# Kernel optimization log

Hardware: AMD Instinct MI355X
Metric: run time of the kernel (lower is better)

The kernel has to match this reference:

```python
import jax, jax.numpy as jnp
import numpy as np

B, T, S, O, U = 512, 1024, 64, 32, 16


def setup_inputs() -> dict:
    key = jax.random.key(0)
    ks = jax.random.split(key, 6)
    obs = jax.random.normal(ks[0], (B, T, O), jnp.float32)
    inputs = jax.random.normal(ks[1], (B, T, U), jnp.float32)
    # Stable transition matrix: spectral radius < 1 so the recursion doesn't blow up
    A = 0.9 * jnp.eye(S, dtype=jnp.float32) + (0.05 / np.sqrt(S)) * jax.random.normal(ks[2], (S, S), jnp.float32)
    B_mat = 0.1 * jax.random.normal(ks[3], (S, U), jnp.float32)
    C = jax.random.normal(ks[4], (O, S), jnp.float32) / np.sqrt(S)
    Q = jnp.eye(S, dtype=jnp.float32)  # module default when Q not provided
    R = jnp.eye(O, dtype=jnp.float32)  # module default when R not provided
    x0 = jax.random.normal(ks[5], (S,), jnp.float32)
    return dict(obs=obs, inputs=inputs, A=A, B_mat=B_mat, C=C, Q=Q, R=R, x0=x0)


def reference(obs, inputs, A, B_mat, C, Q, R, x0):
    b = obs.shape[0]
    s = A.shape[0]
    I_S = jnp.eye(s, dtype=obs.dtype)
    x_init = jnp.broadcast_to(x0, (b, s))            # initial_state_mean repeated over batch
    P_init = jnpp = jnp.broadcast_to(I_S, (b, s, s))  # P[:,0] = I

    def step(carry, zs):
        x, P = carry          # x: [b,S], P: [b,S,S]
        z, u = zs             # z: [b,O], u: [b,U]
        # stage 1: predict
        x_prior = x @ A.T + u @ B_mat.T                       # [b,S]
        P_prior = jnp.einsum('ij,bjk,lk->bil', A, P, A) + Q   # A P A^T + Q
        # stage 2: measurement update
        S_inn = jnp.einsum('ij,bjk,lk->bil', C, P_prior, C) + R   # [b,O,O]
        K = jnp.einsum('bij,kj,bkl->bil', P_prior, C, jnp.linalg.inv(S_inn))  # [b,S,O]
        innov = z - x_prior @ C.T                              # [b,O]
        x_post = x_prior + jnp.einsum('bij,bj->bi', K, innov)  # [b,S]
        P_post = (I_S - jnp.einsum('bij,jk->bik', K, C)) @ P_prior
        return (x_post, P_post), x_post

    xs = (jnp.swapaxes(obs, 0, 1), jnp.swapaxes(inputs, 0, 1))  # time-major
    _, x_seq = jax.lax.scan(step, (x_init, P_init), xs)          # [T,b,S]
    states_est = jnp.concatenate([x_init[:, None, :], jnp.swapaxes(x_seq, 0, 1)], axis=1)  # [b,T+1,S]
    return states_est
```

## Files before the change

kernel.cpp:

```cpp
#include <hip/hip_runtime.h>

#define NS 64
#define NO 32
#define NU 16
#define NT 1024
#define NB 512
#define TCAP 192
#define GROW 112
#define GROW4 28

#define OFF_A    0
#define OFF_AT   4096
#define OFF_C    8192
#define OFF_CT   10240
#define OFF_CA   12288
#define OFF_CB   14336
#define OFF_B    14848
#define OFF_Q    15872
#define OFF_R    19968
#define OFF_P    20992
#define OFF_PP   25088
#define OFF_X    29184
#define OFF_X2   33280
#define OFF_CP   35328
#define OFF_K    37376
#define OFF_DB   39424
#define LDS_FLOATS 39456

#define FMA4(acc, s, v) do { float4 _v = (v); float _s = (s); \
  acc.x = fmaf(_s,_v.x,acc.x); acc.y = fmaf(_s,_v.y,acc.y); \
  acc.z = fmaf(_s,_v.z,acc.z); acc.w = fmaf(_s,_v.w,acc.w); } while(0)
#define FNM4(acc, s, v) do { float4 _v = (v); float _s = -(s); \
  acc.x = fmaf(_s,_v.x,acc.x); acc.y = fmaf(_s,_v.y,acc.y); \
  acc.z = fmaf(_s,_v.z,acc.z); acc.w = fmaf(_s,_v.w,acc.w); } while(0)

#define GJ_STEP(SRC, DST, KK) do { \
  const float* _s = (SRC); float* _d = (DST); const int _k = (KK); \
  float prcp = 1.0f / _s[_k*64 + _k]; \
  float f  = _s[gi*64 + _k] * prcp; \
  float p0 = _s[_k*64 + gj],      p1 = _s[_k*64 + 16 + gj]; \
  float p2 = _s[_k*64 + 32 + gj], p3 = _s[_k*64 + 48 + gj]; \
  float x0 = _s[gi*64 + gj],      x1 = _s[gi*64 + 16 + gj]; \
  float x2 = _s[gi*64 + 32 + gj], x3 = _s[gi*64 + 48 + gj]; \
  bool piv = (gi == _k); \
  _d[gi*64 + gj]      = piv ? x0 : fmaf(-f, p0, x0); \
  _d[gi*64 + 16 + gj] = piv ? x1 : fmaf(-f, p1, x1); \
  _d[gi*64 + 32 + gj] = piv ? x2 : fmaf(-f, p2, x2); \
  _d[gi*64 + 48 + gj] = piv ? x3 : fmaf(-f, p3, x3); \
} while(0)

__global__ __launch_bounds__(512) void riccati_kernel(
    const float* __restrict__ Ag, const float* __restrict__ Bg,
    const float* __restrict__ Cg, const float* __restrict__ Qg,
    const float* __restrict__ Rg, float* __restrict__ Gout,
    int* __restrict__ hdr, int tcap)
{
  extern __shared__ float sm[];
  float* Al  = sm + OFF_A;
  float* Atl = sm + OFF_AT;
  float* Cl  = sm + OFF_C;
  float* CTl = sm + OFF_CT;
  float* CAl = sm + OFF_CA;
  float* CBl = sm + OFF_CB;
  float* Bl  = sm + OFF_B;
  float* Ql  = sm + OFF_Q;
  float* Rl  = sm + OFF_R;
  float* Pl  = sm + OFF_P;
  float* Ppl = sm + OFF_PP;
  float* Xl  = sm + OFF_X;
  float* X2l = sm + OFF_X2;
  float* CPl = sm + OFF_CP;
  float* Kl  = sm + OFF_K;
  float* db  = sm + OFF_DB;
  __shared__ unsigned redmax;
  __shared__ int done;

  const int tid = threadIdx.x;

  for (int x = tid; x < 4096; x += 512) Al[x] = Ag[x];
  for (int x = tid; x < 2048; x += 512) Cl[x] = Cg[x];
  for (int x = tid; x < 1024; x += 512) Bl[x] = Bg[x];
  for (int x = tid; x < 4096; x += 512) Ql[x] = Qg[x];
  for (int x = tid; x < 1024; x += 512) Rl[x] = Rg[x];
  for (int x = tid; x < 4096; x += 512) Pl[x] = ((x >> 6) == (x & 63)) ? 1.f : 0.f;
  for (int x = tid; x < 2048; x += 512) Kl[x] = 0.f;
  if (tid == 0) { redmax = 0u; done = 0; }
  __syncthreads();
  for (int x = tid; x < 4096; x += 512) Atl[(x & 63)*64 + (x >> 6)] = Al[x];
  for (int x = tid; x < 2048; x += 512) CTl[(x & 63)*32 + (x >> 6)] = Cl[x];
  __syncthreads();

  const int r0  = tid >> 4;
  const int r1  = r0 + 32;
  const int j16 = tid & 15;
  const int gi  = r0;
  const int gj  = j16;
  const float4* A4  = (const float4*)Al;
  const float4* At4 = (const float4*)Atl;
  const float4* C4  = (const float4*)Cl;
  const float4* CT4 = (const float4*)CTl;
  const float4* CA4 = (const float4*)CAl;
  const float4* CB4 = (const float4*)CBl;
  const float4* B4  = (const float4*)Bl;
  const float4* Q4  = (const float4*)Ql;
  const float4* R4  = (const float4*)Rl;
  float4* P4   = (float4*)Pl;
  float4* Pp4  = (float4*)Ppl;
  float4* X4   = (float4*)Xl;
  float4* CP4v = (float4*)CPl;
  float4* K4   = (float4*)Kl;

  {
    float4 acc = make_float4(0,0,0,0);
    #pragma unroll 2
    for (int k4 = 0; k4 < 16; ++k4) {
      float4 c = C4[r0*16 + k4];
      FMA4(acc, c.x, A4[(4*k4+0)*16 + j16]);
      FMA4(acc, c.y, A4[(4*k4+1)*16 + j16]);
      FMA4(acc, c.z, A4[(4*k4+2)*16 + j16]);
      FMA4(acc, c.w, A4[(4*k4+3)*16 + j16]);
    }
    ((float4*)CAl)[tid] = acc;
  }
  if (tid < 128) {
    int i = tid >> 2, j4 = tid & 3;
    float4 acc = make_float4(0,0,0,0);
    #pragma unroll 2
    for (int k4 = 0; k4 < 16; ++k4) {
      float4 c = C4[i*16 + k4];
      FMA4(acc, c.x, B4[(4*k4+0)*4 + j4]);
      FMA4(acc, c.y, B4[(4*k4+1)*4 + j4]);
      FMA4(acc, c.z, B4[(4*k4+2)*4 + j4]);
      FMA4(acc, c.w, B4[(4*k4+3)*4 + j4]);
    }
    ((float4*)CBl)[tid] = acc;
  }
  __syncthreads();

  #pragma unroll 1
  for (int t = 0; t < tcap; ++t) {
    {
      float4 acc0 = make_float4(0,0,0,0), acc1 = make_float4(0,0,0,0);
      #pragma unroll 2
      for (int k4 = 0; k4 < 16; ++k4) {
        float4 a0 = A4[r0*16 + k4];
        float4 a1 = A4[r1*16 + k4];
        float4 p0 = P4[(4*k4+0)*16 + j16];
        float4 p1 = P4[(4*k4+1)*16 + j16];
        float4 p2 = P4[(4*k4+2)*16 + j16];
        float4 p3 = P4[(4*k4+3)*16 + j16];
        FMA4(acc0, a0.x, p0); FMA4(acc0, a0.y, p1); FMA4(acc0, a0.z, p2); FMA4(acc0, a0.w, p3);
        FMA4(acc1, a1.x, p0); FMA4(acc1, a1.y, p1); FMA4(acc1, a1.z, p2); FMA4(acc1, a1.w, p3);
      }
      X4[r0*16 + j16] = acc0;
      X4[r1*16 + j16] = acc1;
    }
    __syncthreads();
    {
      float4 acc0 = Q4[r0*16 + j16];
      float4 acc1 = Q4[r1*16 + j16];
      #pragma unroll 2
      for (int k4 = 0; k4 < 16; ++k4) {
        float4 a0 = X4[r0*16 + k4];
        float4 a1 = X4[r1*16 + k4];
        float4 p0 = At4[(4*k4+0)*16 + j16];
        float4 p1 = At4[(4*k4+1)*16 + j16];
        float4 p2 = At4[(4*k4+2)*16 + j16];
        float4 p3 = At4[(4*k4+3)*16 + j16];
        FMA4(acc0, a0.x, p0); FMA4(acc0, a0.y, p1); FMA4(acc0, a0.z, p2); FMA4(acc0, a0.w, p3);
        FMA4(acc1, a1.x, p0); FMA4(acc1, a1.y, p1); FMA4(acc1, a1.z, p2); FMA4(acc1, a1.w, p3);
      }
      Pp4[r0*16 + j16] = acc0;
      Pp4[r1*16 + j16] = acc1;
    }
    __syncthreads();
    {
      float4 acc = make_float4(0,0,0,0);
      #pragma unroll 2
      for (int k4 = 0; k4 < 16; ++k4) {
        float4 c = C4[r0*16 + k4];
        FMA4(acc, c.x, Pp4[(4*k4+0)*16 + j16]);
        FMA4(acc, c.y, Pp4[(4*k4+1)*16 + j16]);
        FMA4(acc, c.z, Pp4[(4*k4+2)*16 + j16]);
        FMA4(acc, c.w, Pp4[(4*k4+3)*16 + j16]);
      }
      CP4v[tid] = acc;
    }
    __syncthreads();
    if (tid < 256) {
      int i = tid >> 3, j4 = tid & 7;
      float4 acc = R4[i*8 + j4];
      #pragma unroll 2
      for (int k4 = 0; k4 < 16; ++k4) {
        float4 c = CP4v[i*16 + k4];
        FMA4(acc, c.x, CT4[(4*k4+0)*8 + j4]);
        FMA4(acc, c.y, CT4[(4*k4+1)*8 + j4]);
        FMA4(acc, c.z, CT4[(4*k4+2)*8 + j4]);
        FMA4(acc, c.w, CT4[(4*k4+3)*8 + j4]);
      }
      X4[i*16 + j4] = acc;
    } else {
      int z = tid - 256;
      int i = z >> 3, j4 = z & 7;
      float4 idv;
      idv.x = (i == j4*4+0) ? 1.f : 0.f;
      idv.y = (i == j4*4+1) ? 1.f : 0.f;
      idv.z = (i == j4*4+2) ? 1.f : 0.f;
      idv.w = (i == j4*4+3) ? 1.f : 0.f;
      X4[i*16 + 8 + j4] = idv;
    }
    __syncthreads();
    #pragma unroll 1
    for (int k = 0; k < 32; k += 2) {
      GJ_STEP(Xl, X2l, k);
      __syncthreads();
      GJ_STEP(X2l, Xl, k + 1);
      __syncthreads();
    }
    if (tid < 32) db[tid] = 1.0f / Xl[tid*64 + tid];
    __syncthreads();
    {
      int i = tid >> 3, j4 = tid & 7;
      float4 acc = make_float4(0,0,0,0);
      #pragma unroll 4
      for (int m = 0; m < 32; ++m) {
        float w = CPl[m*64 + i] * db[m];
        FMA4(acc, w, X4[m*16 + 8 + j4]);
      }
      float4 old = K4[i*8 + j4];
      float d = fmaxf(fmaxf(fabsf(acc.x-old.x), fabsf(acc.y-old.y)),
                      fmaxf(fabsf(acc.z-old.z), fabsf(acc.w-old.w)));
      #pragma unroll
      for (int off = 32; off; off >>= 1) d = fmaxf(d, __shfl_xor(d, off, 64));
      if ((tid & 63) == 0) atomicMax(&redmax, __float_as_uint(d));
      K4[i*8 + j4] = acc;
    }
    __syncthreads();
    float4* Gt = (float4*)Gout + (size_t)t * (64*GROW4);
    {
      float4 accP0 = Pp4[r0*16+j16], accM0 = A4[r0*16+j16];
      float4 accP1 = Pp4[r1*16+j16], accM1 = A4[r1*16+j16];
      #pragma unroll 4
      for (int m = 0; m < 32; ++m) {
        float k0 = Kl[r0*32 + m];
        float k1 = Kl[r1*32 + m];
        float4 cp = CP4v[m*16 + j16];
        float4 ca = CA4[m*16 + j16];
        FNM4(accP0, k0, cp); FNM4(accM0, k0, ca);
        FNM4(accP1, k1, cp); FNM4(accM1, k1, ca);
      }
      P4[r0*16+j16] = accP0;
      P4[r1*16+j16] = accP1;
      Gt[r0*GROW4 + j16] = accM0;
      Gt[r1*GROW4 + j16] = accM1;
    }
    if (tid < 256) {
      int i = tid >> 2, j4 = tid & 3;
      float4 accN = B4[i*4 + j4];
      #pragma unroll 4
      for (int m = 0; m < 32; ++m) FNM4(accN, Kl[i*32 + m], CB4[m*4 + j4]);
      Gt[i*GROW4 + 16 + j4] = accN;
    } else {
      int z = tid - 256;
      int i = z >> 3, j4 = z & 7;
      Gt[i*GROW4 + 20 + j4]      = K4[i*8 + j4];
      Gt[(i+32)*GROW4 + 20 + j4] = K4[(i+32)*8 + j4];
    }
    __syncthreads();
    if (tid == 0) {
      float dmax = __uint_as_float(redmax);
      redmax = 0u;
      if (dmax < 1.5e-4f || t == tcap - 1) { done = 1; hdr[0] = t; }
    }
    __syncthreads();
    if (done) break;
  }
}

#define XSTEP(T, CUR, NXT) do { \
  const int t_ = (T); \
  float uin = 0.f, zin = 0.f; \
  if (t_ + 1 < NT) { \
    if (i < 16)      uin = ins[((size_t)b*NT + t_ + 1)*NU + i]; \
    else if (i < 48) zin = obs[((size_t)b*NT + t_ + 1)*NO + (i - 16)]; \
  } \
  if (t_ <= tconv) { \
    const float4* Gr = (const float4*)G + ((size_t)t_*64 + i)*GROW4; \
    _Pragma("unroll") \
    for (int k = 0; k < GROW4; ++k) g[k] = Gr[k]; \
  } \
  float a0 = 0.f, a1 = 0.f, a2 = 0.f, a3 = 0.f; \
  _Pragma("unroll") \
  for (int k = 0; k < GROW4; k += 4) { \
    float4 v0 = (CUR)[k], v1 = (CUR)[k+1], v2 = (CUR)[k+2], v3 = (CUR)[k+3]; \
    a0 = fmaf(g[k].x,   v0.x, a0); a0 = fmaf(g[k].y,   v0.y, a0); \
    a0 = fmaf(g[k].z,   v0.z, a0); a0 = fmaf(g[k].w,   v0.w, a0); \
    a1 = fmaf(g[k+1].x, v1.x, a1); a1 = fmaf(g[k+1].y, v1.y, a1); \
    a1 = fmaf(g[k+1].z, v1.z, a1); a1 = fmaf(g[k+1].w, v1.w, a1); \
    a2 = fmaf(g[k+2].x, v2.x, a2); a2 = fmaf(g[k+2].y, v2.y, a2); \
    a2 = fmaf(g[k+2].z, v2.z, a2); a2 = fmaf(g[k+2].w, v2.w, a2); \
    a3 = fmaf(g[k+3].x, v3.x, a3); a3 = fmaf(g[k+3].y, v3.y, a3); \
    a3 = fmaf(g[k+3].z, v3.z, a3); a3 = fmaf(g[k+3].w, v3.w, a3); \
  } \
  float acc = (a0 + a1) + (a2 + a3); \
  float* ny = (float*)(NXT); \
  ny[i] = acc; \
  if (i < 16) ny[64 + i] = uin; else if (i < 48) ny[80 + (i - 16)] = zin; \
  out[((size_t)b*(NT+1) + t_ + 1)*NS + i] = acc; \
  __syncthreads(); \
} while(0)

__global__ __launch_bounds__(64) void xrec_kernel(
    const float* __restrict__ obs, const float* __restrict__ ins,
    const float* __restrict__ x0, const float* __restrict__ G,
    const int* __restrict__ hdr, float* __restrict__ out)
{
  const int b = blockIdx.x;
  const int i = threadIdx.x;
  const int tconv = hdr[0];
  __shared__ float4 y4[2][GROW4];
  float* y0 = (float*)y4[0];

  float xi = x0[i];
  y0[i] = xi;
  out[(size_t)b*(NT+1)*NS + i] = xi;
  if (i < 16)      y0[64 + i]        = ins[(size_t)b*NT*NU + i];
  else if (i < 48) y0[80 + (i - 16)] = obs[(size_t)b*NT*NO + (i - 16)];
  __syncthreads();

  float4 g[GROW4];
  #pragma unroll 1
  for (int t = 0; t < NT; t += 2) {
    XSTEP(t,     y4[0], y4[1]);
    XSTEP(t + 1, y4[1], y4[0]);
  }
}

extern "C" void kernel_launch(void* const* d_in, const int* in_sizes, int n_in,
                              void* d_out, int out_size, void* d_ws, size_t ws_size,
                              hipStream_t stream) {
  const float* obs = (const float*)d_in[0];
  const float* ins = (const float*)d_in[1];
  const float* A   = (const float*)d_in[2];
  const float* Bm  = (const float*)d_in[3];
  const float* C   = (const float*)d_in[4];
  const float* Q   = (const float*)d_in[5];
  const float* R   = (const float*)d_in[6];
  const float* x0  = (const float*)d_in[7];
  float* out = (float*)d_out;

  int* hdr = (int*)d_ws;
  float* G = (float*)((char*)d_ws + 256);
  const size_t per_t = (size_t)64 * GROW * sizeof(float);
  int tcap = TCAP;
  if ((size_t)tcap * per_t + 256 > ws_size) tcap = (int)((ws_size - 256) / per_t);
  if (tcap < 1) tcap = 1;

  hipFuncSetAttribute((const void*)riccati_kernel,
                      hipFuncAttributeMaxDynamicSharedMemorySize,
                      LDS_FLOATS * sizeof(float));
  riccati_kernel<<<1, 512, LDS_FLOATS * sizeof(float), stream>>>(
      A, Bm, C, Q, R, G, hdr, tcap);
  xrec_kernel<<<NB, NS, 0, stream>>>(obs, ins, x0, G, hdr, out);
}
```

Baseline: 4.013 ms.

## Chunk the time recurrence into parallel segments with block scan and correction

The sequential per-batch state recurrence is split into 16 time chunks that run in parallel from zero initial state. A block scan then propagates chunk boundary states using a precomputed 64th power of the converged closed-loop matrix, and a correction kernel adds the propagated homogeneous response to each chunk. The Riccati kernel also swaps Gauss-Jordan inversion for warm-started Newton-Schulz iterations, loosens the convergence threshold and cap, and computes the matrix power by repeated squaring. Looser convergence and iterative inversion risk accuracy, and the extra kernels add launches and a read-modify-write pass over the output.

```diff
diff --git a/kernel.cpp b/kernel.cpp
--- a/kernel.cpp
+++ b/kernel.cpp
@@ -5,9 +5,18 @@
 #define NU 16
 #define NT 1024
 #define NB 512
-#define TCAP 192
+#define TCAP 64
+#define NCH 16
 #define GROW 112
 #define GROW4 28
+
+#define WS_G    256
+#define WS_G_SZ (64*64*112*4)
+#define WS_M64  (WS_G + WS_G_SZ)
+#define WS_D    (WS_M64 + 16384)
+#define WS_D_SZ (NCH*NB*NS*4)
+#define NEED_FULL (WS_D + WS_D_SZ)
+#define NEED_G    (WS_G + WS_G_SZ)
 
 #define OFF_A    0
 #define OFF_AT   4096
@@ -16,16 +25,17 @@
 #define OFF_CA   12288
 #define OFF_CB   14336
 #define OFF_B    14848
-#define OFF_Q    15872
-#define OFF_R    19968
-#define OFF_P    20992
-#define OFF_PP   25088
-#define OFF_X    29184
-#define OFF_X2   33280
-#define OFF_CP   35328
-#define OFF_K    37376
-#define OFF_DB   39424
-#define LDS_FLOATS 39456
+#define OFF_R    15872
+#define OFF_P    16896
+#define OFF_PP   20992
+#define OFF_X    25088
+#define OFF_CP   29184
+#define OFF_K    31232
+#define OFF_S    33280
+#define OFF_XA   34432
+#define OFF_XB   35584
+#define OFF_E    36736
+#define LDS_FLOATS 37888
 
 #define FMA4(acc, s, v) do { float4 _v = (v); float _s = (s); \
   acc.x = fmaf(_s,_v.x,acc.x); acc.y = fmaf(_s,_v.y,acc.y); \
@@ -34,26 +44,11 @@
   acc.x = fmaf(_s,_v.x,acc.x); acc.y = fmaf(_s,_v.y,acc.y); \
   acc.z = fmaf(_s,_v.z,acc.z); acc.w = fmaf(_s,_v.w,acc.w); } while(0)
 
-#define GJ_STEP(SRC, DST, KK) do { \
-  const float* _s = (SRC); float* _d = (DST); const int _k = (KK); \
-  float prcp = 1.0f / _s[_k*64 + _k]; \
-  float f  = _s[gi*64 + _k] * prcp; \
-  float p0 = _s[_k*64 + gj],      p1 = _s[_k*64 + 16 + gj]; \
-  float p2 = _s[_k*64 + 32 + gj], p3 = _s[_k*64 + 48 + gj]; \
-  float x0 = _s[gi*64 + gj],      x1 = _s[gi*64 + 16 + gj]; \
-  float x2 = _s[gi*64 + 32 + gj], x3 = _s[gi*64 + 48 + gj]; \
-  bool piv = (gi == _k); \
-  _d[gi*64 + gj]      = piv ? x0 : fmaf(-f, p0, x0); \
-  _d[gi*64 + 16 + gj] = piv ? x1 : fmaf(-f, p1, x1); \
-  _d[gi*64 + 32 + gj] = piv ? x2 : fmaf(-f, p2, x2); \
-  _d[gi*64 + 48 + gj] = piv ? x3 : fmaf(-f, p3, x3); \
-} while(0)
-
 __global__ __launch_bounds__(512) void riccati_kernel(
     const float* __restrict__ Ag, const float* __restrict__ Bg,
     const float* __restrict__ Cg, const float* __restrict__ Qg,
     const float* __restrict__ Rg, float* __restrict__ Gout,
-    int* __restrict__ hdr, int tcap)
+    float* __restrict__ M64g, int* __restrict__ hdr, int tcap)
 {
   extern __shared__ float sm[];
   float* Al  = sm + OFF_A;
@@ -63,16 +58,17 @@
   float* CAl = sm + OFF_CA;
   float* CBl = sm + OFF_CB;
   float* Bl  = sm + OFF_B;
-  float* Ql  = sm + OFF_Q;
   float* Rl  = sm + OFF_R;
   float* Pl  = sm + OFF_P;
   float* Ppl = sm + OFF_PP;
   float* Xl  = sm + OFF_X;
-  float* X2l = sm + OFF_X2;
   float* CPl = sm + OFF_CP;
   float* Kl  = sm + OFF_K;
-  float* db  = sm + OFF_DB;
-  __shared__ unsigned redmax;
+  float* Sl  = sm + OFF_S;
+  float* Xa_ = sm + OFF_XA;
+  float* Xb_ = sm + OFF_XB;
+  float* El  = sm + OFF_E;
+  __shared__ unsigned redmax, lmax_u;
   __shared__ int done;
 
   const int tid = threadIdx.x;
@@ -80,11 +76,10 @@
   for (int x = tid; x < 4096; x += 512) Al[x] = Ag[x];
   for (int x = tid; x < 2048; x += 512) Cl[x] = Cg[x];
   for (int x = tid; x < 1024; x += 512) Bl[x] = Bg[x];
-  for (int x = tid; x < 4096; x += 512) Ql[x] = Qg[x];
   for (int x = tid; x < 1024; x += 512) Rl[x] = Rg[x];
   for (int x = tid; x < 4096; x += 512) Pl[x] = ((x >> 6) == (x & 63)) ? 1.f : 0.f;
   for (int x = tid; x < 2048; x += 512) Kl[x] = 0.f;
-  if (tid == 0) { redmax = 0u; done = 0; }
+  if (tid == 0) { redmax = 0u; lmax_u = 0u; done = 0; }
   __syncthreads();
   for (int x = tid; x < 4096; x += 512) Atl[(x & 63)*64 + (x >> 6)] = Al[x];
   for (int x = tid; x < 2048; x += 512) CTl[(x & 63)*32 + (x >> 6)] = Cl[x];
@@ -93,8 +88,6 @@
   const int r0  = tid >> 4;
   const int r1  = r0 + 32;
   const int j16 = tid & 15;
-  const int gi  = r0;
-  const int gj  = j16;
   const float4* A4  = (const float4*)Al;
   const float4* At4 = (const float4*)Atl;
   const float4* C4  = (const float4*)Cl;
@@ -102,7 +95,7 @@
   const float4* CA4 = (const float4*)CAl;
   const float4* CB4 = (const float4*)CBl;
   const float4* B4  = (const float4*)Bl;
-  const float4* Q4  = (const float4*)Ql;
+  const float4* Q4  = (const float4*)Qg;
   const float4* R4  = (const float4*)Rl;
   float4* P4   = (float4*)Pl;
   float4* Pp4  = (float4*)Ppl;
@@ -198,35 +191,56 @@
         FMA4(acc, c.z, CT4[(4*k4+2)*8 + j4]);
         FMA4(acc, c.w, CT4[(4*k4+3)*8 + j4]);
       }
-      X4[i*16 + j4] = acc;
-    } else {
-      int z = tid - 256;
-      int i = z >> 3, j4 = z & 7;
-      float4 idv;
-      idv.x = (i == j4*4+0) ? 1.f : 0.f;
-      idv.y = (i == j4*4+1) ? 1.f : 0.f;
-      idv.z = (i == j4*4+2) ? 1.f : 0.f;
-      idv.w = (i == j4*4+3) ? 1.f : 0.f;
-      X4[i*16 + 8 + j4] = idv;
-    }
-    __syncthreads();
-    #pragma unroll 1
-    for (int k = 0; k < 32; k += 2) {
-      GJ_STEP(Xl, X2l, k);
+      ((float4*)Sl)[i*9 + j4] = acc;
+    }
+    __syncthreads();
+    if (t == 0) {
+      if (tid < 32) {
+        float s = 0.f;
+        #pragma unroll 4
+        for (int k = 0; k < 32; ++k) s += fabsf(Sl[tid*36 + k]);
+        atomicMax(&lmax_u, __float_as_uint(s));
+      }
       __syncthreads();
-      GJ_STEP(X2l, Xl, k + 1);
+      float inv = 1.0f / __uint_as_float(lmax_u);
+      for (int x = tid; x < 1024; x += 512) {
+        int r = x >> 5, cc = x & 31;
+        Xa_[r*36 + cc] = (r == cc) ? inv : 0.f;
+      }
       __syncthreads();
     }
-    if (tid < 32) db[tid] = 1.0f / Xl[tid*64 + tid];
-    __syncthreads();
+    {
+      int nsteps = (t == 0) ? 12 : (t < 3 ? 8 : (t < 8 ? 4 : 2));
+      float* Xc = Xa_;
+      float* Xn = Xb_;
+      #pragma unroll 1
+      for (int it = 0; it < nsteps; ++it) {
+        if (tid < 256) {
+          int i = tid >> 3, j4 = tid & 7;
+          float4 acc = make_float4(0,0,0,0);
+          #pragma unroll 4
+          for (int k = 0; k < 32; ++k) FMA4(acc, Sl[i*36 + k], ((float4*)Xc)[k*9 + j4]);
+          ((float4*)El)[i*9 + j4] = acc;
+        }
+        __syncthreads();
+        if (tid < 256) {
+          int i = tid >> 3, j4 = tid & 7;
+          float4 x2 = ((float4*)Xc)[i*9 + j4];
+          float4 acc = make_float4(2.f*x2.x, 2.f*x2.y, 2.f*x2.z, 2.f*x2.w);
+          #pragma unroll 4
+          for (int k = 0; k < 32; ++k) FNM4(acc, Xc[i*36 + k], ((float4*)El)[k*9 + j4]);
+          ((float4*)Xn)[i*9 + j4] = acc;
+        }
+        __syncthreads();
+        float* tmp = Xc; Xc = Xn; Xn = tmp;
+      }
+    }
     {
       int i = tid >> 3, j4 = tid & 7;
+      const float4* Si4 = (const float4*)Xa_;
       float4 acc = make_float4(0,0,0,0);
       #pragma unroll 4
-      for (int m = 0; m < 32; ++m) {
-        float w = CPl[m*64 + i] * db[m];
-        FMA4(acc, w, X4[m*16 + 8 + j4]);
-      }
+      for (int m = 0; m < 32; ++m) FMA4(acc, CPl[m*64 + i], Si4[m*9 + j4]);
       float4 old = K4[i*8 + j4];
       float d = fmaxf(fmaxf(fabsf(acc.x-old.x), fabsf(acc.y-old.y)),
                       fmaxf(fabsf(acc.z-old.z), fabsf(acc.w-old.w)));
@@ -234,6 +248,12 @@
       for (int off = 32; off; off >>= 1) d = fmaxf(d, __shfl_xor(d, off, 64));
       if ((tid & 63) == 0) atomicMax(&redmax, __float_as_uint(d));
       K4[i*8 + j4] = acc;
+    }
+    __syncthreads();
+    if (tid == 0) {
+      float dmax = __uint_as_float(redmax);
+      redmax = 0u;
+      if (dmax < 6e-4f || t == tcap - 1) { done = 1; hdr[0] = t; }
     }
     __syncthreads();
     float4* Gt = (float4*)Gout + (size_t)t * (64*GROW4);
@@ -253,6 +273,10 @@
       P4[r1*16+j16] = accP1;
       Gt[r0*GROW4 + j16] = accM0;
       Gt[r1*GROW4 + j16] = accM1;
+      if (done) {
+        X4[r0*16 + j16] = accM0;
+        X4[r1*16 + j16] = accM1;
+      }
     }
     if (tid < 256) {
       int i = tid >> 2, j4 = tid & 3;
@@ -267,13 +291,170 @@
       Gt[(i+32)*GROW4 + 20 + j4] = K4[(i+32)*8 + j4];
     }
     __syncthreads();
-    if (tid == 0) {
-      float dmax = __uint_as_float(redmax);
-      redmax = 0u;
-      if (dmax < 1.5e-4f || t == tcap - 1) { done = 1; hdr[0] = t; }
-    }
-    __syncthreads();
     if (done) break;
+  }
+
+  float* S_ = Xl;
+  float* D_ = Ppl;
+  #pragma unroll 1
+  for (int q = 0; q < 6; ++q) {
+    const float4* s4 = (const float4*)S_;
+    float4 acc0 = make_float4(0,0,0,0), acc1 = make_float4(0,0,0,0);
+    #pragma unroll 2
+    for (int k4 = 0; k4 < 16; ++k4) {
+      float4 a0 = s4[r0*16 + k4];
+      float4 a1 = s4[r1*16 + k4];
+      float4 p0 = s4[(4*k4+0)*16 + j16];
+      float4 p1 = s4[(4*k4+1)*16 + j16];
+      float4 p2 = s4[(4*k4+2)*16 + j16];
+      float4 p3 = s4[(4*k4+3)*16 + j16];
+      FMA4(acc0, a0.x, p0); FMA4(acc0, a0.y, p1); FMA4(acc0, a0.z, p2); FMA4(acc0, a0.w, p3);
+      FMA4(acc1, a1.x, p0); FMA4(acc1, a1.y, p1); FMA4(acc1, a1.z, p2); FMA4(acc1, a1.w, p3);
+    }
+    __syncthreads();
+    ((float4*)D_)[r0*16 + j16] = acc0;
+    ((float4*)D_)[r1*16 + j16] = acc1;
+    __syncthreads();
+    float* tmp = S_; S_ = D_; D_ = tmp;
+  }
+  for (int x = tid; x < 4096; x += 512) M64g[x] = S_[x];
+}
+
+#define CSTEP(KK, CUR, NXT) do { \
+  const int k_ = (KK); const int t_ = t0 + k_; \
+  float uin = 0.f, zin = 0.f; \
+  if (k_ + 1 < 64) { \
+    if (i < 16)      uin = ins[((size_t)b*NT + t_ + 1)*NU + i]; \
+    else if (i < 48) zin = obs[((size_t)b*NT + t_ + 1)*NO + (i - 16)]; \
+  } \
+  if (cz && t_ <= tconv) { \
+    const float4* Gr = (const float4*)G + ((size_t)t_*64 + i)*GROW4; \
+    _Pragma("unroll") \
+    for (int k = 0; k < GROW4; ++k) g[k] = Gr[k]; \
+  } \
+  float a0 = 0.f, a1 = 0.f, a2 = 0.f, a3 = 0.f; \
+  _Pragma("unroll") \
+  for (int k = 0; k < GROW4; k += 4) { \
+    float4 v0 = (CUR)[k], v1 = (CUR)[k+1], v2 = (CUR)[k+2], v3 = (CUR)[k+3]; \
+    a0 = fmaf(g[k].x,   v0.x, a0); a0 = fmaf(g[k].y,   v0.y, a0); \
+    a0 = fmaf(g[k].z,   v0.z, a0); a0 = fmaf(g[k].w,   v0.w, a0); \
+    a1 = fmaf(g[k+1].x, v1.x, a1); a1 = fmaf(g[k+1].y, v1.y, a1); \
+    a1 = fmaf(g[k+1].z, v1.z, a1); a1 = fmaf(g[k+1].w, v1.w, a1); \
+    a2 = fmaf(g[k+2].x, v2.x, a2); a2 = fmaf(g[k+2].y, v2.y, a2); \
+    a2 = fmaf(g[k+2].z, v2.z, a2); a2 = fmaf(g[k+2].w, v2.w, a2); \
+    a3 = fmaf(g[k+3].x, v3.x, a3); a3 = fmaf(g[k+3].y, v3.y, a3); \
+    a3 = fmaf(g[k+3].z, v3.z, a3); a3 = fmaf(g[k+3].w, v3.w, a3); \
+  } \
+  float acc = (a0 + a1) + (a2 + a3); \
+  float* ny = (float*)(NXT); \
+  ny[i] = acc; \
+  if (i < 16) ny[64 + i] = uin; else if (i < 48) ny[80 + (i - 16)] = zin; \
+  out[((size_t)b*(NT+1) + t_ + 1)*NS + i] = acc; \
+  __syncthreads(); \
+} while(0)
+
+__global__ __launch_bounds__(64) void chunk_kernel(
+    const float* __restrict__ obs, const float* __restrict__ ins,
+    const float* __restrict__ x0, const float* __restrict__ G,
+    const int* __restrict__ hdr, float* __restrict__ out,
+    float* __restrict__ Dws)
+{
+  const int c = blockIdx.x;
+  const int b = blockIdx.y;
+  const int i = threadIdx.x;
+  const int tconv = hdr[0];
+  const bool cz = (c == 0);
+  const int t0 = c * 64;
+  __shared__ float4 y4[2][GROW4];
+  float* y0 = (float*)y4[0];
+  float4 g[GROW4];
+
+  if (cz) {
+    float xi = x0[i];
+    y0[i] = xi;
+    out[(size_t)b*(NT+1)*NS + i] = xi;
+  } else {
+    y0[i] = 0.f;
+    const float4* Gr = (const float4*)G + ((size_t)tconv*64 + i)*GROW4;
+    #pragma unroll
+    for (int k = 0; k < GROW4; ++k) g[k] = Gr[k];
+  }
+  if (i < 16)      y0[64 + i]        = ins[((size_t)b*NT + t0)*NU + i];
+  else if (i < 48) y0[80 + (i - 16)] = obs[((size_t)b*NT + t0)*NO + (i - 16)];
+  __syncthreads();
+
+  #pragma unroll 1
+  for (int k = 0; k < 64; k += 2) {
+    CSTEP(k,     y4[0], y4[1]);
+    CSTEP(k + 1, y4[1], y4[0]);
+  }
+  Dws[((size_t)c*NB + b)*NS + i] = ((float*)y4[0])[i];
+}
+
+__global__ __launch_bounds__(64) void bscan_kernel(
+    const float* __restrict__ M64g, float* __restrict__ Dws)
+{
+  const int b = blockIdx.x;
+  const int i = threadIdx.x;
+  __shared__ float sv[64];
+  float4 m[16];
+  const float4* M4 = (const float4*)M64g + i*16;
+  #pragma unroll
+  for (int k = 0; k < 16; ++k) m[k] = M4[k];
+  float s = Dws[(size_t)b*NS + i];
+  #pragma unroll 1
+  for (int c = 1; c < NCH; ++c) {
+    sv[i] = s;
+    __syncthreads();
+    float d = Dws[((size_t)c*NB + b)*NS + i];
+    Dws[((size_t)c*NB + b)*NS + i] = s;
+    const float4* cv = (const float4*)sv;
+    float a0=0.f, a1=0.f, a2=0.f, a3=0.f;
+    #pragma unroll
+    for (int q = 0; q < 16; q += 4) {
+      float4 y0=cv[q], y1=cv[q+1], y2=cv[q+2], y3=cv[q+3];
+      a0=fmaf(m[q].x,y0.x,a0);   a0=fmaf(m[q].y,y0.y,a0);   a0=fmaf(m[q].z,y0.z,a0);   a0=fmaf(m[q].w,y0.w,a0);
+      a1=fmaf(m[q+1].x,y1.x,a1); a1=fmaf(m[q+1].y,y1.y,a1); a1=fmaf(m[q+1].z,y1.z,a1); a1=fmaf(m[q+1].w,y1.w,a1);
+      a2=fmaf(m[q+2].x,y2.x,a2); a2=fmaf(m[q+2].y,y2.y,a2); a2=fmaf(m[q+2].z,y2.z,a2); a2=fmaf(m[q+2].w,y2.w,a2);
+      a3=fmaf(m[q+3].x,y3.x,a3); a3=fmaf(m[q+3].y,y3.y,a3); a3=fmaf(m[q+3].z,y3.z,a3); a3=fmaf(m[q+3].w,y3.w,a3);
+    }
+    s = ((a0+a1)+(a2+a3)) + d;
+    __syncthreads();
+  }
+}
+
+__global__ __launch_bounds__(64) void corr_kernel(
+    const float* __restrict__ G, const int* __restrict__ hdr,
+    const float* __restrict__ Dws, float* __restrict__ out)
+{
+  const int c = blockIdx.x + 1;
+  const int b = blockIdx.y;
+  const int i = threadIdx.x;
+  const int tconv = hdr[0];
+  __shared__ float sv[2][64];
+  float4 m[16];
+  const float4* Mr = (const float4*)(G + ((size_t)tconv*64 + i)*GROW);
+  #pragma unroll
+  for (int k = 0; k < 16; ++k) m[k] = Mr[k];
+  sv[0][i] = Dws[((size_t)c*NB + b)*NS + i];
+  __syncthreads();
+  float* outb = out + ((size_t)b*(NT+1) + (size_t)c*64)*NS;
+  #pragma unroll 1
+  for (int k = 1; k <= 64; ++k) {
+    const float4* cv = (const float4*)sv[(k-1)&1];
+    float a0=0.f, a1=0.f, a2=0.f, a3=0.f;
+    #pragma unroll
+    for (int q = 0; q < 16; q += 4) {
+      float4 y0=cv[q], y1=cv[q+1], y2=cv[q+2], y3=cv[q+3];
+      a0=fmaf(m[q].x,y0.x,a0);   a0=fmaf(m[q].y,y0.y,a0);   a0=fmaf(m[q].z,y0.z,a0);   a0=fmaf(m[q].w,y0.w,a0);
+      a1=fmaf(m[q+1].x,y1.x,a1); a1=fmaf(m[q+1].y,y1.y,a1); a1=fmaf(m[q+1].z,y1.z,a1); a1=fmaf(m[q+1].w,y1.w,a1);
+      a2=fmaf(m[q+2].x,y2.x,a2); a2=fmaf(m[q+2].y,y2.y,a2); a2=fmaf(m[q+2].z,y2.z,a2); a2=fmaf(m[q+2].w,y2.w,a2);
+      a3=fmaf(m[q+3].x,y3.x,a3); a3=fmaf(m[q+3].y,y3.y,a3); a3=fmaf(m[q+3].z,y3.z,a3); a3=fmaf(m[q+3].w,y3.w,a3);
+    }
+    float nv = (a0+a1)+(a2+a3);
+    sv[k&1][i] = nv;
+    outb[(size_t)k*NS + i] += nv;
+    __syncthreads();
   }
 }
 
@@ -349,17 +530,29 @@
   const float* x0  = (const float*)d_in[7];
   float* out = (float*)d_out;
 
-  int* hdr = (int*)d_ws;
-  float* G = (float*)((char*)d_ws + 256);
-  const size_t per_t = (size_t)64 * GROW * sizeof(float);
+  int*   hdr  = (int*)d_ws;
+  float* G    = (float*)((char*)d_ws + WS_G);
+  float* M64g = (float*)((char*)d_ws + WS_M64);
+  float* Dws  = (float*)((char*)d_ws + WS_D);
+
   int tcap = TCAP;
-  if ((size_t)tcap * per_t + 256 > ws_size) tcap = (int)((ws_size - 256) / per_t);
-  if (tcap < 1) tcap = 1;
+  if (ws_size < (size_t)NEED_G) {
+    size_t per_t = (size_t)64 * GROW * sizeof(float);
+    tcap = (int)((ws_size - 256) / per_t);
+    if (tcap < 1) tcap = 1;
+  }
 
   hipFuncSetAttribute((const void*)riccati_kernel,
                       hipFuncAttributeMaxDynamicSharedMemorySize,
                       LDS_FLOATS * sizeof(float));
   riccati_kernel<<<1, 512, LDS_FLOATS * sizeof(float), stream>>>(
-      A, Bm, C, Q, R, G, hdr, tcap);
-  xrec_kernel<<<NB, NS, 0, stream>>>(obs, ins, x0, G, hdr, out);
+      A, Bm, C, Q, R, G, M64g, hdr, tcap);
+
+  if (ws_size >= (size_t)NEED_FULL) {
+    chunk_kernel<<<dim3(NCH, NB), 64, 0, stream>>>(obs, ins, x0, G, hdr, out, Dws);
+    bscan_kernel<<<NB, 64, 0, stream>>>(M64g, Dws);
+    corr_kernel<<<dim3(NCH - 1, NB), 64, 0, stream>>>(G, hdr, Dws, out);
+  } else {
+    xrec_kernel<<<NB, 64, 0, stream>>>(obs, ins, x0, G, hdr, out);
+  }
 }
```

New measurement: 3.273 ms. 18.5% less time.
